# Performance work log

Measured on AMD Instinct MI355X. Metric: run time of the kernel, lower is better.

## Reference

```python
import jax, jax.numpy as jnp
import numpy as np

B, S_IMG, S_TXT, D, H, HD = 1, 2048, 512, 3072, 24, 128
A_TOK, A_DIM = 4, 1024
S_TOT = S_IMG + S_TXT
EPS = 1e-6
SCALE = 1.0


def _heads(x):
    # [B, S, D] -> [B, H, S, HD]
    return x.reshape(B, -1, H, HD).transpose(0, 2, 1, 3)


def _rms(x, w):
    return x * jax.lax.rsqrt(jnp.mean(x * x, axis=-1, keepdims=True) + EPS) * w


def _rope(x, cos, sin):
    # diffusers apply_rotary_emb, use_real=True, use_real_unbind_dim=-1
    xr = x.reshape(*x.shape[:-1], HD // 2, 2)
    x1, x2 = xr[..., 0], xr[..., 1]
    x_rot = jnp.stack([-x2, x1], axis=-1).reshape(x.shape)
    return x * cos + x_rot * sin


def _sdpa(q, k, v):
    scores = jnp.einsum('bhqd,bhkd->bhqk', q, k) / np.sqrt(HD).astype(np.float32)
    return jnp.einsum('bhqk,bhkd->bhqd', jax.nn.softmax(scores, axis=-1), v)


def setup_inputs() -> dict:
    key = jax.random.key(0)
    ks = jax.random.split(key, 24)
    s = 0.02
    inp = {
        'hidden_states': jax.random.normal(ks[0], (B, S_IMG, D), jnp.float32),
        'encoder_hidden_states': jax.random.normal(ks[1], (B, S_TXT, D), jnp.float32),
        'adapter_embeds': jax.random.normal(ks[2], (B, A_TOK, A_DIM), jnp.float32),
        'freqs_cos': jnp.cos(jax.random.normal(ks[3], (S_TOT, HD), jnp.float32)),
        'freqs_sin': jnp.sin(jax.random.normal(ks[3], (S_TOT, HD), jnp.float32)),
        'Wq': jax.random.normal(ks[4], (D, D), jnp.float32) * s,
        'bq': jnp.zeros((D,), jnp.float32),
        'Wk': jax.random.normal(ks[5], (D, D), jnp.float32) * s,
        'bk': jnp.zeros((D,), jnp.float32),
        'Wv': jax.random.normal(ks[6], (D, D), jnp.float32) * s,
        'bv': jnp.zeros((D,), jnp.float32),
        'norm_q_w': jnp.ones((HD,), jnp.float32),
        'norm_k_w': jnp.ones((HD,), jnp.float32),
        'Wq_add': jax.random.normal(ks[7], (D, D), jnp.float32) * s,
        'bq_add': jnp.zeros((D,), jnp.float32),
        'Wk_add': jax.random.normal(ks[8], (D, D), jnp.float32) * s,
        'bk_add': jnp.zeros((D,), jnp.float32),
        'Wv_add': jax.random.normal(ks[9], (D, D), jnp.float32) * s,
        'bv_add': jnp.zeros((D,), jnp.float32),
        'norm_added_q_w': jnp.ones((HD,), jnp.float32),
        'norm_added_k_w': jnp.ones((HD,), jnp.float32),
        'Wo': jax.random.normal(ks[10], (D, D), jnp.float32) * s,
        'bo': jnp.zeros((D,), jnp.float32),
        'Wo_add': jax.random.normal(ks[11], (D, D), jnp.float32) * s,
        'bo_add': jnp.zeros((D,), jnp.float32),
        'Wk_adapt': jax.random.normal(ks[12], (A_DIM, D), jnp.float32) * s,
        'Wv_adapt': jax.random.normal(ks[13], (A_DIM, D), jnp.float32) * s,
        'block_scaler': jnp.ones((1,), jnp.float32),
    }
    return inp


def reference(hidden_states, encoder_hidden_states, adapter_embeds, freqs_cos, freqs_sin,
              Wq, bq, Wk, bk, Wv, bv, norm_q_w, norm_k_w,
              Wq_add, bq_add, Wk_add, bk_add, Wv_add, bv_add,
              norm_added_q_w, norm_added_k_w, Wo, bo, Wo_add, bo_add,
              Wk_adapt, Wv_adapt, block_scaler):
    # image-token Q/K/V + per-head RMSNorm
    q = _rms(_heads(hidden_states @ Wq + bq), norm_q_w)
    k = _rms(_heads(hidden_states @ Wk + bk), norm_k_w)
    v = _heads(hidden_states @ Wv + bv)
    # text-token Q/K/V + per-head RMSNorm
    eq = _rms(_heads(encoder_hidden_states @ Wq_add + bq_add), norm_added_q_w)
    ek = _rms(_heads(encoder_hidden_states @ Wk_add + bk_add), norm_added_k_w)
    ev = _heads(encoder_hidden_states @ Wv_add + bv_add)
    # joint sequence: [text, image]
    q = jnp.concatenate([eq, q], axis=2)
    k = jnp.concatenate([ek, k], axis=2)
    v = jnp.concatenate([ev, v], axis=2)
    # RoPE on full joint sequence
    q = _rope(q, freqs_cos, freqs_sin)
    k = _rope(k, freqs_cos, freqs_sin)
    # main joint attention
    hs = _sdpa(q, k, v)                                    # [B,H,S_TOT,HD]
    hs = hs.transpose(0, 2, 1, 3).reshape(B, S_TOT, D)
    # adapter cross-attention (vision-direct branch)
    vd_k = _heads(adapter_embeds @ Wk_adapt)               # [B,H,A_TOK,HD]
    vd_v = _heads(adapter_embeds @ Wv_adapt)
    vd = _sdpa(q, vd_k, vd_v)
    vd = vd.transpose(0, 2, 1, 3).reshape(B, S_TOT, D)
    hs = hs + SCALE * (vd * block_scaler)
    # split back and project
    enc_out = hs[:, :S_TXT] @ Wo_add + bo_add
    img_out = hs[:, S_TXT:] @ Wo + bo
    return img_out, enc_out
```

## Files before the change

### kernel.cpp

```cpp
#include <hip/hip_runtime.h>

typedef unsigned short u16;
typedef short s16x8 __attribute__((ext_vector_type(8)));
typedef float f32x4 __attribute__((ext_vector_type(4)));

#define S_TXTC 512
#define S_TOTC 2560
#define DM 3072
#define NH 24
#define HDM 128

__device__ __forceinline__ float b2f(u16 u){ unsigned int i = ((unsigned int)u)<<16; float f; __builtin_memcpy(&f,&i,4); return f; }
__device__ __forceinline__ u16 f2b(float f){ unsigned int i; __builtin_memcpy(&i,&f,4); unsigned int r = i + 0x7FFFu + ((i>>16)&1u); return (u16)(r>>16); }
__device__ __forceinline__ unsigned int pk2(float lo, float hi){
  return (unsigned int)f2b(lo) | ((unsigned int)f2b(hi)<<16);
}
__device__ __forceinline__ s16x8 pk8(float4 a, float4 b){
  s16x8 r;
  r[0]=(short)f2b(a.x); r[1]=(short)f2b(a.y); r[2]=(short)f2b(a.z); r[3]=(short)f2b(a.w);
  r[4]=(short)f2b(b.x); r[5]=(short)f2b(b.y); r[6]=(short)f2b(b.z); r[7]=(short)f2b(b.w);
  return r;
}
__device__ __forceinline__ void g2l16(const void* g, void* l){
  __builtin_amdgcn_global_load_lds((const __attribute__((address_space(1))) void*)g,
                                   (__attribute__((address_space(3))) void*)l, 16, 0, 0);
}
__device__ __forceinline__ float fexp2(float x){ return __builtin_amdgcn_exp2f(x); }

__global__ __launch_bounds__(256) void fillv(float* __restrict__ p, int n, float v){
  int i = blockIdx.x*256 + threadIdx.x;
  if (i < n) p[i] = v;
}

__global__ __launch_bounds__(256) void castbias(const float* __restrict__ a, const float* __restrict__ b,
    u16* __restrict__ dst, int na8, int n8,
    const float* __restrict__ b0, const float* __restrict__ b1, const float* __restrict__ b2,
    const float* __restrict__ c0, const float* __restrict__ c1, const float* __restrict__ c2,
    float* __restrict__ bdst){
  int blk = blockIdx.x;
  if (blk < 3840){
    int i = blk*256 + threadIdx.x;
    if (i >= n8) return;
    const float* src = (i < na8)? a + (size_t)i*8 : b + (size_t)(i-na8)*8;
    float4 f0 = *(const float4*)src;
    float4 f1 = *(const float4*)(src+4);
    *(s16x8*)(dst + (size_t)i*8) = pk8(f0,f1);
  } else {
    int i = (blk-3840)*256 + threadIdx.x;
    if (i >= 18432) return;
    int j = (i < 9216)? i : i - 9216;
    const float* s0 = (i<9216)? b0 : c0; const float* s1 = (i<9216)? b1 : c1; const float* s2 = (i<9216)? b2 : c2;
    bdst[i] = (j<3072)? s0[j] : (j<6144? s1[j-3072] : s2[j-6144]);
  }
}

__global__ __launch_bounds__(256) void ktrans3(const float* __restrict__ W0, const float* __restrict__ W1,
    const float* __restrict__ W2, u16* __restrict__ D0, u16* __restrict__ D1, u16* __restrict__ D2){
  const float* W = (blockIdx.z==0)? W0 : ((blockIdx.z==1)? W1 : W2);
  u16* Wt = (blockIdx.z==0)? D0 : ((blockIdx.z==1)? D1 : D2);
  __shared__ __align__(16) u16 t[64*72];
  int nt = blockIdx.x*64, kt_ = blockIdx.y*64;
  int tid = threadIdx.x;
  #pragma unroll
  for (int i=0;i<2;i++){
    int q = tid + 256*i;
    int r = q>>3, c8 = (q&7)*8;
    float4 f0 = *(const float4*)(W + (size_t)(kt_+r)*DM + nt + c8);
    float4 f1 = *(const float4*)(W + (size_t)(kt_+r)*DM + nt + c8 + 4);
    *(s16x8*)&t[r*72 + c8] = pk8(f0,f1);
  }
  __syncthreads();
  #pragma unroll
  for (int i=0;i<2;i++){
    int q = tid + 256*i;
    int n = q>>3, k8 = (q&7)*8;
    s16x8 v;
    #pragma unroll
    for (int j=0;j<8;j++) v[j] = (short)t[(k8+j)*72 + n];
    *(s16x8*)(Wt + (size_t)(nt+n)*DM + kt_ + k8) = v;
  }
}

template<int OUT32>
__device__ __forceinline__ void gcore(u16* la, u16* lb,
    const u16* __restrict__ A, const u16* __restrict__ Bt,
    const float* __restrict__ bias, void* __restrict__ Cv,
    int ldc, int rb, int crb, int cb){
  const int K = DM;
  int tid = threadIdx.x, w = tid>>6, l = tid&63, g = l>>4, c16 = l&15;
  int wr = (w>>1)*64, wc = (w&1)*64;
  f32x4 acc[4][4] = {};
  const u16* aL = A  + (size_t)(rb + w*32 + (l>>2))*K + (l&3)*8;
  const u16* bL = Bt + (size_t)(cb + w*32 + (l>>2))*K + (l&3)*8;
  u16* laB = la + w*1024;
  u16* lbB = lb + w*1024;
  for (int ks=0; ks<K; ks+=32){
    g2l16(aL + ks,                laB);
    g2l16(aL + 16*(size_t)K + ks, laB + 512);
    g2l16(bL + ks,                lbB);
    g2l16(bL + 16*(size_t)K + ks, lbB + 512);
    __syncthreads();
    s16x8 af[4], bf[4];
    #pragma unroll
    for (int m=0;m<4;m++) af[m] = *(const s16x8*)&la[(wr + m*16 + c16)*32 + g*8];
    #pragma unroll
    for (int n=0;n<4;n++) bf[n] = *(const s16x8*)&lb[(wc + n*16 + c16)*32 + g*8];
    #pragma unroll
    for (int m=0;m<4;m++)
      #pragma unroll
      for (int n=0;n<4;n++)
        acc[m][n] = __builtin_amdgcn_mfma_f32_16x16x32_bf16(af[m], bf[n], acc[m][n], 0,0,0);
    __syncthreads();
  }
  #pragma unroll
  for (int n=0;n<4;n++){
    int col = cb + wc + n*16 + c16;
    float bv = bias[col];
    #pragma unroll
    for (int m=0;m<4;m++){
      int r0 = crb + wr + m*16 + g*4;
      #pragma unroll
      for (int r=0;r<4;r++){
        float oo = acc[m][n][r] + bv;
        if (OUT32) ((float*)Cv)[(size_t)(r0+r)*ldc + col] = oo;
        else       ((u16*)Cv)[(size_t)(r0+r)*ldc + col] = f2b(oo);
      }
    }
  }
}

__device__ __forceinline__ void xcd_swz(int& bx, int& by){
  int gx = gridDim.x, nwg = gx*gridDim.y;
  int id = blockIdx.y*gx + blockIdx.x;
  int q = nwg>>3;
  int nid = (id&7)*q + (id>>3);
  bx = nid % gx; by = nid / gx;
}

__global__ __launch_bounds__(256) void qkv_gemm(const u16* __restrict__ A, const u16* __restrict__ Bt,
                                                const float* __restrict__ bias, u16* __restrict__ C){
  __shared__ __align__(16) u16 la[4096];
  __shared__ __align__(16) u16 lb[4096];
  int bx, by; xcd_swz(bx, by);
  gcore<0>(la, lb, A, Bt, bias, C, 3*DM, bx*128, bx*128, by*128);
}

__global__ __launch_bounds__(256) void out_gemm(const u16* __restrict__ hsb,
    const u16* __restrict__ woT, const u16* __restrict__ woaT,
    const float* __restrict__ bo, const float* __restrict__ boa, float* __restrict__ out){
  __shared__ __align__(16) u16 la[4096];
  __shared__ __align__(16) u16 lb[4096];
  int bx, by; xcd_swz(bx, by);
  bool txt = (bx < 4);
  int rb = bx*128;
  const u16* Bt = txt? woaT : woT;
  const float* bias = txt? boa : bo;
  float* dst = txt? out + (size_t)2048*DM : out;
  int crb = txt? rb : rb - 512;
  gcore<1>(la, lb, hsb, Bt, bias, dst, DM, rb, crb, by*128);
}

__global__ __launch_bounds__(256) void epi_fused(
    const u16* __restrict__ qkvI, const u16* __restrict__ qkvT,
    const float* __restrict__ nqw, const float* __restrict__ nkw,
    const float* __restrict__ naq, const float* __restrict__ nak,
    const float* __restrict__ fcos, const float* __restrict__ fsin,
    u16* __restrict__ qh, u16* __restrict__ kh, u16* __restrict__ vt,
    const float* __restrict__ ad, const float* __restrict__ Wkad, const float* __restrict__ Wvad,
    u16* __restrict__ vdk, u16* __restrict__ vdv){
  __shared__ __align__(16) u16 t[64*136];
  int blk = blockIdx.x;
  if (blk < 30720){
    int wid = blk*4 + (threadIdx.x>>6);
    int lane = threadIdx.x&63;
    int which = wid / (NH*S_TOTC);
    int rem = wid % (NH*S_TOTC);
    int h = rem / S_TOTC, tok = rem % S_TOTC;
    const u16* src = ((tok<S_TXTC)? qkvT + (size_t)tok*(3*DM) : qkvI + (size_t)(tok-S_TXTC)*(3*DM))
                     + which*DM + h*HDM;
    const float* nw = which? ((tok<S_TXTC)? nak : nkw) : ((tok<S_TXTC)? naq : nqw);
    int d = lane*2;
    unsigned int u = *(const unsigned int*)(src + d);
    float x0 = b2f((u16)(u&0xffffu)), x1 = b2f((u16)(u>>16));
    float ss = x0*x0 + x1*x1;
    #pragma unroll
    for (int m=1;m<64;m<<=1) ss += __shfl_xor(ss, m);
    float rr = rsqrtf(ss*(1.f/128.f) + 1e-6f);
    float y0 = x0*rr*nw[d];
    float y1 = x1*rr*nw[d+1];
    float2 cc = *(const float2*)(fcos + (size_t)tok*HDM + d);
    float2 sn = *(const float2*)(fsin + (size_t)tok*HDM + d);
    float sc = which? 1.0f : 0.1275174436f;
    float o0 = (y0*cc.x - y1*sn.x)*sc;
    float o1 = (y1*cc.y + y0*sn.y)*sc;
    u16* dst = (which? kh : qh) + ((size_t)h*S_TOTC + tok)*HDM + d;
    *(unsigned int*)dst = pk2(o0, o1);
  } else if (blk < 31680){
    int bv = blk - 30720;
    int h = bv % NH, tb = bv / NH;
    int tok0 = tb*64, tid = threadIdx.x;
    #pragma unroll
    for (int i=0;i<4;i++){
      int q = tid + 256*i;
      int tr = q>>4, c8 = (q&15)*8;
      int tok = tok0 + tr;
      const u16* src = ((tok<S_TXTC)? qkvT + (size_t)tok*(3*DM) : qkvI + (size_t)(tok-S_TXTC)*(3*DM))
                       + 2*DM + h*HDM;
      *(s16x8*)&t[tr*136 + c8] = *(const s16x8*)(src + c8);
    }
    __syncthreads();
    #pragma unroll
    for (int i=0;i<4;i++){
      int q = tid + 256*i;
      int d = q>>3, j8 = (q&7)*8;
      s16x8 v;
      #pragma unroll
      for (int j=0;j<8;j++) v[j] = (short)t[(j8+j)*136 + d];
      *(s16x8*)(vt + ((size_t)h*HDM + d)*S_TOTC + tok0 + j8) = v;
    }
  } else {
    int bv = blk - 31680;
    int tensor = bv / 48;
    int col = (bv % 48)*64 + (threadIdx.x & 63);
    int tok = threadIdx.x >> 6;
    const float* Wp = tensor? Wvad : Wkad;
    const float* arow = ad + tok*1024;
    float s = 0.f;
    #pragma unroll 4
    for (int k=0;k<1024;k++)
      s += arow[k] * Wp[(size_t)k*DM + col];
    int hh = col>>7, d = col&127;
    (tensor? vdv : vdk)[(hh*4+tok)*HDM + d] = f2b(s);
  }
}

__global__ __launch_bounds__(512,2) void attnk(const u16* __restrict__ qh, const u16* __restrict__ kh,
    const u16* __restrict__ vt, const u16* __restrict__ vdk, const u16* __restrict__ vdv,
    const float* __restrict__ bscale, u16* __restrict__ hs){
  __shared__ __align__(16) u16 kts[2][64*128];
  __shared__ __align__(16) u16 vts[2][128*64];
  __shared__ __align__(16) u16 pwb[128*64];
  int h = blockIdx.y, qb = blockIdx.x*128;
  int tid = threadIdx.x, w = tid>>6, l = tid&63, g = l>>4, c16 = l&15;
  int qrow = qb + w*16 + c16;
  int c7 = c16&7;
  s16x8 qf[4];
  #pragma unroll
  for (int kc=0;kc<4;kc++) qf[kc] = *(const s16x8*)(qh + ((size_t)h*S_TOTC + qrow)*HDM + kc*32 + g*8);
  f32x4 acc[8];
  #pragma unroll
  for (int dt=0;dt<8;dt++) acc[dt] = f32x4{0.f,0.f,0.f,0.f};
  float m_[4] = {-3e38f,-3e38f,-3e38f,-3e38f};
  float l_[4] = {0.f,0.f,0.f,0.f};
  const u16* khB = kh + (size_t)h*S_TOTC*HDM;
  const u16* vtB = vt + (size_t)h*HDM*S_TOTC;

  auto STAGE = [&](int buf, int kb){
    #pragma unroll
    for (int c=0;c<2;c++){
      int krow = w*8 + c*4 + (l>>4);
      int kchunk = (l&15) ^ (krow&7);
      g2l16(khB + (size_t)(kb + krow)*HDM + kchunk*8, &kts[buf][w*1024 + c*512]);
      int vrow = w*16 + c*8 + (l>>3);
      int vchunk = (l&7) ^ (vrow&7);
      g2l16(vtB + (size_t)vrow*S_TOTC + kb + vchunk*8, &vts[buf][w*1024 + c*512]);
    }
  };
  auto COMPUTE = [&](int buf){
    f32x4 s[4];
    #pragma unroll
    for (int su=0;su<4;su++) s[su] = f32x4{0.f,0.f,0.f,0.f};
    __builtin_amdgcn_s_setprio(1);
    #pragma unroll
    for (int su=0;su<4;su++)
      #pragma unroll
      for (int kc=0;kc<4;kc++){
        s16x8 kf = *(const s16x8*)&kts[buf][(su*16+c16)*128 + ((kc*4+g) ^ c7)*8];
        s[su] = __builtin_amdgcn_mfma_f32_16x16x32_bf16(qf[kc], kf, s[su], 0,0,0);
      }
    __builtin_amdgcn_s_setprio(0);
    float tm[4];
    #pragma unroll
    for (int r=0;r<4;r++)
      tm[r] = fmaxf(fmaxf(s[0][r],s[1][r]), fmaxf(s[2][r],s[3][r]));
    #pragma unroll
    for (int m=1;m<16;m<<=1)
      #pragma unroll
      for (int r=0;r<4;r++) tm[r] = fmaxf(tm[r], __shfl_xor(tm[r], m));
    bool need = !__all(tm[0]<=m_[0]+11.5415603f && tm[1]<=m_[1]+11.5415603f &&
                       tm[2]<=m_[2]+11.5415603f && tm[3]<=m_[3]+11.5415603f);
    if (need){
      float corr[4];
      #pragma unroll
      for (int r=0;r<4;r++){
        float mn = fmaxf(m_[r], tm[r]);
        corr[r] = fexp2(m_[r]-mn);
        m_[r] = mn;
        l_[r] *= corr[r];
      }
      #pragma unroll
      for (int dt=0;dt<8;dt++)
        #pragma unroll
        for (int r=0;r<4;r++) acc[dt][r] *= corr[r];
    }
    float rs[4];
    #pragma unroll
    for (int r=0;r<4;r++){
      rs[r] = 0.f;
      #pragma unroll
      for (int su=0;su<4;su++){ s[su][r] = fexp2(s[su][r]-m_[r]); rs[r] += s[su][r]; }
    }
    #pragma unroll
    for (int m=1;m<16;m<<=1)
      #pragma unroll
      for (int r=0;r<4;r++) rs[r] += __shfl_xor(rs[r], m);
    #pragma unroll
    for (int r=0;r<4;r++) l_[r] += rs[r];
    #pragma unroll
    for (int su=0;su<4;su++){
      int kslot = su*2 + (c16>>3);
      #pragma unroll
      for (int r=0;r<4;r++){
        int prow = w*16 + g*4 + r;
        pwb[prow*64 + (kslot ^ (prow&7))*8 + c7] = f2b(s[su][r]);
      }
    }
    int prow = w*16 + c16;
    s16x8 pf0 = *(const s16x8*)&pwb[prow*64 + ((0+g) ^ c7)*8];
    s16x8 pf1 = *(const s16x8*)&pwb[prow*64 + ((4+g) ^ c7)*8];
    __builtin_amdgcn_s_setprio(1);
    #pragma unroll
    for (int dt=0;dt<8;dt++){
      int vrow = dt*16 + c16;
      s16x8 vf0 = *(const s16x8*)&vts[buf][vrow*64 + ((0+g) ^ c7)*8];
      acc[dt] = __builtin_amdgcn_mfma_f32_16x16x32_bf16(pf0, vf0, acc[dt], 0,0,0);
      s16x8 vf1 = *(const s16x8*)&vts[buf][vrow*64 + ((4+g) ^ c7)*8];
      acc[dt] = __builtin_amdgcn_mfma_f32_16x16x32_bf16(pf1, vf1, acc[dt], 0,0,0);
    }
    __builtin_amdgcn_s_setprio(0);
  };

  STAGE(0, 0);
  __syncthreads();
  int cur = 0;
  for (int kb=0; kb<S_TOTC; kb+=64){
    if (kb+64 < S_TOTC) STAGE(cur^1, kb+64);
    COMPUTE(cur);
    __syncthreads();
    cur ^= 1;
  }

  if (tid < 64){
    int row = tid>>4, slot = (tid&15) ^ (row&7);
    *(s16x8*)&kts[0][row*128 + slot*8] = *(const s16x8*)(vdk + (h*4+(tid>>4))*HDM + (tid&15)*8);
  } else if (tid < 192){
    int d = tid - 64;
    int sl0 = (d&7)*8;
    #pragma unroll
    for (int key=0;key<4;key++) vts[0][d*64 + sl0 + key] = vdv[(h*4+key)*HDM + d];
  }
  __syncthreads();
  f32x4 s2 = {0.f,0.f,0.f,0.f};
  #pragma unroll
  for (int kc=0;kc<4;kc++){
    s16x8 kf = *(const s16x8*)&kts[0][c16*128 + ((kc*4+g) ^ c7)*8];
    s2 = __builtin_amdgcn_mfma_f32_16x16x32_bf16(qf[kc], kf, s2, 0,0,0);
  }
  bool valid = (c16 < 4);
  float m2[4], l2[4];
  #pragma unroll
  for (int r=0;r<4;r++) m2[r] = valid? s2[r] : -3e38f;
  #pragma unroll
  for (int m=1;m<16;m<<=1)
    #pragma unroll
    for (int r=0;r<4;r++) m2[r] = fmaxf(m2[r], __shfl_xor(m2[r], m));
  #pragma unroll
  for (int r=0;r<4;r++){ float p = valid? fexp2(s2[r]-m2[r]) : 0.f; s2[r]=p; l2[r]=p; }
  #pragma unroll
  for (int m=1;m<16;m<<=1)
    #pragma unroll
    for (int r=0;r<4;r++) l2[r] += __shfl_xor(l2[r], m);
  #pragma unroll
  for (int r=0;r<4;r++){
    int prow = w*16 + g*4 + r;
    int s0 = (c16>>3) ^ (prow&7);
    int s1 = (2 + (c16>>3)) ^ (prow&7);
    pwb[prow*64 + s0*8 + c7] = f2b(s2[r]);
    pwb[prow*64 + s1*8 + c7] = (u16)0;
  }
  int prow2 = w*16 + c16;
  s16x8 pf2 = *(const s16x8*)&pwb[prow2*64 + (g ^ c7)*8];
  f32x4 a2[8];
  #pragma unroll
  for (int dt=0;dt<8;dt++) a2[dt] = f32x4{0.f,0.f,0.f,0.f};
  #pragma unroll
  for (int dt=0;dt<8;dt++){
    int vrow = dt*16 + c16;
    s16x8 vf = *(const s16x8*)&vts[0][vrow*64 + (g ^ c7)*8];
    a2[dt] = __builtin_amdgcn_mfma_f32_16x16x32_bf16(pf2, vf, a2[dt], 0,0,0);
  }
  float sb = bscale[0];
  float rl[4], rl2[4];
  #pragma unroll
  for (int r=0;r<4;r++){ rl[r] = 1.f/l_[r]; rl2[r] = sb/l2[r]; }
  #pragma unroll
  for (int dt=0;dt<8;dt++)
    #pragma unroll
    for (int r=0;r<4;r++){
      int tok = qb + w*16 + g*4 + r;
      int col = h*HDM + dt*16 + c16;
      hs[(size_t)tok*DM + col] = f2b(acc[dt][r]*rl[r] + a2[dt][r]*rl2[r]);
    }
}

extern "C" void kernel_launch(void* const* d_in, const int* in_sizes, int n_in,
                              void* d_out, int out_size, void* d_ws, size_t ws_size,
                              hipStream_t stream){
  static const int expect[28] = {
    6291456, 1572864, 4096, 327680, 327680,
    9437184, 3072, 9437184, 3072, 9437184, 3072, 128, 128,
    9437184, 3072, 9437184, 3072, 9437184, 3072, 128, 128,
    9437184, 3072, 9437184, 3072, 3145728, 3145728, 1 };
  bool ok = (n_in == 28);
  if (ok) for (int i=0;i<28;i++) if (in_sizes[i] != expect[i]) { ok = false; break; }
  if (!ok){ fillv<<<(out_size+255)/256,256,0,stream>>>((float*)d_out, out_size, 7.0f); return; }
  if (ws_size < 119611392ull){ fillv<<<(out_size+255)/256,256,0,stream>>>((float*)d_out, out_size, 9.0f); return; }

  const float* hidden = (const float*)d_in[0];
  const float* enc    = (const float*)d_in[1];
  const float* adapt  = (const float*)d_in[2];
  const float* fcos   = (const float*)d_in[3];
  const float* fsin   = (const float*)d_in[4];
  const float* Wq  = (const float*)d_in[5];  const float* bq  = (const float*)d_in[6];
  const float* Wk  = (const float*)d_in[7];  const float* bk  = (const float*)d_in[8];
  const float* Wv  = (const float*)d_in[9];  const float* bv  = (const float*)d_in[10];
  const float* nqw = (const float*)d_in[11]; const float* nkw = (const float*)d_in[12];
  const float* Wqa = (const float*)d_in[13]; const float* bqa = (const float*)d_in[14];
  const float* Wka = (const float*)d_in[15]; const float* bka = (const float*)d_in[16];
  const float* Wva = (const float*)d_in[17]; const float* bva = (const float*)d_in[18];
  const float* naq = (const float*)d_in[19]; const float* nak = (const float*)d_in[20];
  const float* Wo  = (const float*)d_in[21]; const float* bo  = (const float*)d_in[22];
  const float* Woa = (const float*)d_in[23]; const float* boa = (const float*)d_in[24];
  const float* Wkad = (const float*)d_in[25]; const float* Wvad = (const float*)d_in[26];
  const float* bsc  = (const float*)d_in[27];
  float* out = (float*)d_out;

  char* ws = (char*)d_ws;
  u16* wt3   = (u16*)(ws);
  u16* kh    = (u16*)(ws);
  u16* vth   = (u16*)(ws + 15728640);
  u16* vdk   = (u16*)(ws + 31457280);
  u16* vdv   = (u16*)(ws + 31481856);
  u16* woaT  = (u16*)(ws + 33554432);
  u16* hbf   = (u16*)(ws + 56623104);
  u16* qh    = (u16*)(ws + 56623104);
  u16* qkvI  = (u16*)(ws + 72351744);
  u16* hsb   = (u16*)(ws + 72351744);
  u16* woT   = (u16*)(ws + 88080384);
  u16* qkvT  = (u16*)(ws + 110100480);
  float* biasA = (float*)(ws + 119537664);
  float* biasB = (float*)(ws + 119574528);

  castbias<<<3912,256,0,stream>>>(hidden, enc, hbf, 786432, 983040,
                                  bq,bk,bv, bqa,bka,bva, biasA);
  ktrans3<<<dim3(48,48,3),256,0,stream>>>(Wq, Wk, Wv, wt3, wt3 + (size_t)DM*DM, wt3 + (size_t)2*DM*DM);
  qkv_gemm<<<dim3(16,72),256,0,stream>>>(hbf, wt3, biasA, qkvI);
  ktrans3<<<dim3(48,48,3),256,0,stream>>>(Wqa, Wka, Wva, wt3, wt3 + (size_t)DM*DM, wt3 + (size_t)2*DM*DM);
  qkv_gemm<<<dim3(4,72),256,0,stream>>>(hbf + (size_t)2048*DM, wt3, biasB, qkvT);
  epi_fused<<<31776,256,0,stream>>>(qkvI, qkvT, nqw,nkw,naq,nak, fcos,fsin, qh, kh, vth,
                                    adapt, Wkad, Wvad, vdk, vdv);
  attnk<<<dim3(20,24),512,0,stream>>>(qh, kh, vth, vdk, vdv, bsc, hsb);
  ktrans3<<<dim3(48,48,2),256,0,stream>>>(Wo, Woa, Woa, woT, woaT, woaT);
  out_gemm<<<dim3(20,24),256,0,stream>>>(hsb, woT, woaT, bo, boa, out);
}
```

Measured before the change: 671.6 us.

## Widen Q/K norm-RoPE epilogue to half-wave per row and drop setprio in attention

The RMSNorm+RoPE part of the fused epilogue now handles each head row with 32 lanes doing 4 elements each, instead of 64 lanes doing 2. Loads and stores become 8/16-byte vectors, the shuffle reduction is one step shorter, and the block count for that phase is halved. Separately, the s_setprio raises around the MFMA sections in the attention kernel are removed, which changes wave scheduling priority in the main loop.

```diff
diff --git a/kernel.cpp b/kernel.cpp
--- a/kernel.cpp
+++ b/kernel.cpp
@@ -170,33 +170,37 @@
     u16* __restrict__ vdk, u16* __restrict__ vdv){
   __shared__ __align__(16) u16 t[64*136];
   int blk = blockIdx.x;
-  if (blk < 30720){
-    int wid = blk*4 + (threadIdx.x>>6);
+  if (blk < 15360){
     int lane = threadIdx.x&63;
-    int which = wid / (NH*S_TOTC);
-    int rem = wid % (NH*S_TOTC);
+    int rowid = blk*8 + (threadIdx.x>>6)*2 + (lane>>5);
+    int which = rowid / (NH*S_TOTC);
+    int rem = rowid % (NH*S_TOTC);
     int h = rem / S_TOTC, tok = rem % S_TOTC;
     const u16* src = ((tok<S_TXTC)? qkvT + (size_t)tok*(3*DM) : qkvI + (size_t)(tok-S_TXTC)*(3*DM))
                      + which*DM + h*HDM;
     const float* nw = which? ((tok<S_TXTC)? nak : nkw) : ((tok<S_TXTC)? naq : nqw);
-    int d = lane*2;
-    unsigned int u = *(const unsigned int*)(src + d);
-    float x0 = b2f((u16)(u&0xffffu)), x1 = b2f((u16)(u>>16));
-    float ss = x0*x0 + x1*x1;
-    #pragma unroll
-    for (int m=1;m<64;m<<=1) ss += __shfl_xor(ss, m);
+    int d = (lane&31)*4;
+    uint2 u = *(const uint2*)(src + d);
+    float x0 = b2f((u16)(u.x&0xffffu)), x1 = b2f((u16)(u.x>>16));
+    float x2 = b2f((u16)(u.y&0xffffu)), x3 = b2f((u16)(u.y>>16));
+    float ss = x0*x0 + x1*x1 + x2*x2 + x3*x3;
+    #pragma unroll
+    for (int m=1;m<32;m<<=1) ss += __shfl_xor(ss, m);
     float rr = rsqrtf(ss*(1.f/128.f) + 1e-6f);
-    float y0 = x0*rr*nw[d];
-    float y1 = x1*rr*nw[d+1];
-    float2 cc = *(const float2*)(fcos + (size_t)tok*HDM + d);
-    float2 sn = *(const float2*)(fsin + (size_t)tok*HDM + d);
+    float4 nv = *(const float4*)(nw + d);
+    float y0 = x0*rr*nv.x, y1 = x1*rr*nv.y, y2 = x2*rr*nv.z, y3 = x3*rr*nv.w;
+    float4 cc = *(const float4*)(fcos + (size_t)tok*HDM + d);
+    float4 sn = *(const float4*)(fsin + (size_t)tok*HDM + d);
     float sc = which? 1.0f : 0.1275174436f;
     float o0 = (y0*cc.x - y1*sn.x)*sc;
     float o1 = (y1*cc.y + y0*sn.y)*sc;
+    float o2 = (y2*cc.z - y3*sn.z)*sc;
+    float o3 = (y3*cc.w + y2*sn.w)*sc;
     u16* dst = (which? kh : qh) + ((size_t)h*S_TOTC + tok)*HDM + d;
-    *(unsigned int*)dst = pk2(o0, o1);
-  } else if (blk < 31680){
-    int bv = blk - 30720;
+    uint2 ov; ov.x = pk2(o0,o1); ov.y = pk2(o2,o3);
+    *(uint2*)dst = ov;
+  } else if (blk < 16320){
+    int bv = blk - 15360;
     int h = bv % NH, tb = bv / NH;
     int tok0 = tb*64, tid = threadIdx.x;
     #pragma unroll
@@ -219,7 +223,7 @@
       *(s16x8*)(vt + ((size_t)h*HDM + d)*S_TOTC + tok0 + j8) = v;
     }
   } else {
-    int bv = blk - 31680;
+    int bv = blk - 16320;
     int tensor = bv / 48;
     int col = (bv % 48)*64 + (threadIdx.x & 63);
     int tok = threadIdx.x >> 6;
@@ -270,7 +274,6 @@
     f32x4 s[4];
     #pragma unroll
     for (int su=0;su<4;su++) s[su] = f32x4{0.f,0.f,0.f,0.f};
-    __builtin_amdgcn_s_setprio(1);
     #pragma unroll
     for (int su=0;su<4;su++)
       #pragma unroll
@@ -278,7 +281,6 @@
         s16x8 kf = *(const s16x8*)&kts[buf][(su*16+c16)*128 + ((kc*4+g) ^ c7)*8];
         s[su] = __builtin_amdgcn_mfma_f32_16x16x32_bf16(qf[kc], kf, s[su], 0,0,0);
       }
-    __builtin_amdgcn_s_setprio(0);
     float tm[4];
     #pragma unroll
     for (int r=0;r<4;r++)
@@ -328,7 +330,6 @@
     int prow = w*16 + c16;
     s16x8 pf0 = *(const s16x8*)&pwb[prow*64 + ((0+g) ^ c7)*8];
     s16x8 pf1 = *(const s16x8*)&pwb[prow*64 + ((4+g) ^ c7)*8];
-    __builtin_amdgcn_s_setprio(1);
     #pragma unroll
     for (int dt=0;dt<8;dt++){
       int vrow = dt*16 + c16;
@@ -337,7 +338,6 @@
       s16x8 vf1 = *(const s16x8*)&vts[buf][vrow*64 + ((4+g) ^ c7)*8];
       acc[dt] = __builtin_amdgcn_mfma_f32_16x16x32_bf16(pf1, vf1, acc[dt], 0,0,0);
     }
-    __builtin_amdgcn_s_setprio(0);
   };
 
   STAGE(0, 0);
@@ -467,7 +467,7 @@
   qkv_gemm<<<dim3(16,72),256,0,stream>>>(hbf, wt3, biasA, qkvI);
   ktrans3<<<dim3(48,48,3),256,0,stream>>>(Wqa, Wka, Wva, wt3, wt3 + (size_t)DM*DM, wt3 + (size_t)2*DM*DM);
   qkv_gemm<<<dim3(4,72),256,0,stream>>>(hbf + (size_t)2048*DM, wt3, biasB, qkvT);
-  epi_fused<<<31776,256,0,stream>>>(qkvI, qkvT, nqw,nkw,naq,nak, fcos,fsin, qh, kh, vth,
+  epi_fused<<<16416,256,0,stream>>>(qkvI, qkvT, nqw,nkw,naq,nak, fcos,fsin, qh, kh, vth,
                                     adapt, Wkad, Wvad, vdk, vdv);
   attnk<<<dim3(20,24),512,0,stream>>>(qh, kh, vth, vdk, vdv, bsc, hsb);
   ktrans3<<<dim3(48,48,2),256,0,stream>>>(Wo, Woa, Woa, woT, woaT, woaT);
```

After: 666.6 us. No clear change (-0.7%).
